# Performance work log

Hardware: AMD Instinct MI355X
Metric: run time of the kernel (lower is better)

The kernel has to match this reference:

```python
import jax, jax.numpy as jnp
import numpy as np

S = 7  # YOLOv1 grid size


def _iou(a, b):
    # a, b: [..., 4] corner boxes (x1, y1, x2, y2); eps matches global get_iou (1e-7)
    xl = jnp.maximum(a[..., 0], b[..., 0])
    yt = jnp.maximum(a[..., 1], b[..., 1])
    xr = jnp.minimum(a[..., 2], b[..., 2])
    yb = jnp.minimum(a[..., 3], b[..., 3])
    ix = jnp.maximum(xr - xl, 0.0)
    iy = jnp.maximum(yb - yt, 0.0)
    inter = ix * iy
    aa = jnp.abs((a[..., 2] - a[..., 0]) * (a[..., 3] - a[..., 1]))
    ba = jnp.abs((b[..., 2] - b[..., 0]) * (b[..., 3] - b[..., 1]))
    return inter / (aa + ba - inter + 1e-7)


def setup_inputs() -> dict:
    key = jax.random.key(0)
    k1, k2, k3 = jax.random.split(key, 3)
    N, C = 8192, 30  # 5 * num_bboxes(2) + num_classes(20)
    modely = jax.random.normal(k1, (N, S, S, C), dtype=jnp.float32)
    targety = jax.random.uniform(k2, (N, S, S, C), dtype=jnp.float32)
    # keep target wh strictly positive so sqrt(target_wh) is well-behaved
    targety = targety.at[..., 2:4].set(targety[..., 2:4] * 0.9 + 0.05)
    obj = (jax.random.uniform(k3, (N, S, S)) < 0.3).astype(jnp.float32)
    targety = targety.at[..., 4].set(obj)
    targety = targety.at[..., 9].set(obj)
    return {"modely": modely, "targety": targety}


def reference(modely, targety):
    p, t = modely, targety
    # lt_norm: meshgrid 'xy' -> lt[i, j] = (j, i) / S
    cell_x, cell_y = np.meshgrid(np.arange(S), np.arange(S))
    lt = jnp.asarray(np.dstack([cell_x, cell_y]).astype(np.float32)) / S  # [7,7,2]

    coord = (t[..., 4] > 0).astype(p.dtype)   # [N,7,7]
    noobj = (t[..., 4] == 0).astype(p.dtype)  # [N,7,7]

    # predicted box 1: corners from center-offset/size parametrization
    p_xy1 = lt + p[..., 0:2] / S - p[..., 2:4] / 2
    b1 = jnp.concatenate([p_xy1, p[..., 2:4] + p_xy1], axis=-1)
    # predicted box 2: faithfully replicates the source (uses p[...,5:7]/2, not p[...,7:9]/2)
    p_xy2 = lt + p[..., 5:7] * (1.0 / S - 0.5)
    b2 = jnp.concatenate([p_xy2, p[..., 7:9] + p_xy2], axis=-1)
    # target box
    t_xy = lt + t[..., 0:2] / S - t[..., 2:4] / 2
    tb = jnp.concatenate([t_xy, t[..., 2:4] + t_xy], axis=-1)

    iou1 = _iou(b1, tb)  # [N,7,7]
    iou2 = _iou(b2, tb)
    sel = (iou1 >= iou2)[..., None]
    # best box (raw network values, like modely[coord_mask][:, :10][high_bbox])
    box = jnp.where(sel, p[..., 0:5], p[..., 5:10])  # [N,7,7,5]

    xy_se = jnp.sum(coord * jnp.sum((box[..., 0:2] - t[..., 0:2]) ** 2, axis=-1))
    wh_p = jnp.sign(box[..., 2:4]) * jnp.sqrt(jnp.abs(box[..., 2:4]))
    wh_se = jnp.sum(coord * jnp.sum((wh_p - jnp.sqrt(t[..., 2:4])) ** 2, axis=-1))
    obj_se = jnp.sum(coord * (jnp.maximum(iou1, iou2) - box[..., 4]) ** 2)
    noobj_se = jnp.sum(noobj * ((p[..., 4] - t[..., 4]) ** 2 + (p[..., 9] - t[..., 9]) ** 2))
    label_se = jnp.sum(coord * jnp.sum((p[..., 10:] - t[..., 10:]) ** 2, axis=-1))

    loss = 5.0 * (xy_se + wh_se) + obj_se + 0.5 * noobj_se + label_se
    return loss / t.shape[0]
```

## Files before the change

kernel.cpp:

```cpp
#include <hip/hip_runtime.h>


#define NCH 30
#define CELLS_PER_SAMPLE 49

__device__ __forceinline__ float iou_f(float a0, float a1, float a2, float a3,
                                       float b0, float b1, float b2, float b3) {
    float xl = fmaxf(a0, b0);
    float yt = fmaxf(a1, b1);
    float xr = fminf(a2, b2);
    float yb = fminf(a3, b3);
    float ix = fmaxf(xr - xl, 0.0f);
    float iy = fmaxf(yb - yt, 0.0f);
    float inter = ix * iy;
    float aa = fabsf((a2 - a0) * (a3 - a1));
    float ba = fabsf((b2 - b0) * (b3 - b1));
    return inter / (aa + ba - inter + 1e-7f);
}

__device__ __forceinline__ float cell_loss_f(const float* __restrict__ pv,
                                             const float* __restrict__ tv,
                                             int cell) {
    int rem = cell % CELLS_PER_SAMPLE;
    int ci = rem / 7;
    int cj = rem % 7;

    float ltx = (float)cj / 7.0f;
    float lty = (float)ci / 7.0f;

    float coord = (tv[4] > 0.0f) ? 1.0f : 0.0f;
    float noobj = (tv[4] == 0.0f) ? 1.0f : 0.0f;

    float b1x1 = ltx + pv[0] / 7.0f - pv[2] * 0.5f;
    float b1y1 = lty + pv[1] / 7.0f - pv[3] * 0.5f;
    float b1x2 = pv[2] + b1x1;
    float b1y2 = pv[3] + b1y1;

    const float C2 = (float)(1.0 / 7.0 - 0.5);
    float b2x1 = ltx + pv[5] * C2;
    float b2y1 = lty + pv[6] * C2;
    float b2x2 = pv[7] + b2x1;
    float b2y2 = pv[8] + b2y1;

    float tbx1 = ltx + tv[0] / 7.0f - tv[2] * 0.5f;
    float tby1 = lty + tv[1] / 7.0f - tv[3] * 0.5f;
    float tbx2 = tv[2] + tbx1;
    float tby2 = tv[3] + tby1;

    float iou1 = iou_f(b1x1, b1y1, b1x2, b1y2, tbx1, tby1, tbx2, tby2);
    float iou2 = iou_f(b2x1, b2y1, b2x2, b2y2, tbx1, tby1, tbx2, tby2);

    bool sel = (iou1 >= iou2);
    float bx = sel ? pv[0] : pv[5];
    float by = sel ? pv[1] : pv[6];
    float bw = sel ? pv[2] : pv[7];
    float bh = sel ? pv[3] : pv[8];
    float bc = sel ? pv[4] : pv[9];

    float dx = bx - tv[0];
    float dy = by - tv[1];
    float xy_se = dx * dx + dy * dy;

    float sw = (bw > 0.0f) ? 1.0f : ((bw < 0.0f) ? -1.0f : 0.0f);
    float sh = (bh > 0.0f) ? 1.0f : ((bh < 0.0f) ? -1.0f : 0.0f);
    float dw = sw * sqrtf(fabsf(bw)) - sqrtf(tv[2]);
    float dh = sh * sqrtf(fabsf(bh)) - sqrtf(tv[3]);
    float wh_se = dw * dw + dh * dh;

    float mio = fmaxf(iou1, iou2);
    float dob = mio - bc;
    float obj_se = dob * dob;

    float d4 = pv[4] - tv[4];
    float d9 = pv[9] - tv[9];
    float noobj_se = d4 * d4 + d9 * d9;

    float lab = 0.0f;
    #pragma unroll
    for (int k = 10; k < NCH; ++k) {
        float d = pv[k] - tv[k];
        lab += d * d;
    }

    return coord * (5.0f * (xy_se + wh_se) + obj_se + lab)
         + 0.5f * noobj * noobj_se;
}

__global__ __launch_bounds__(256, 4) void yolo_loss_kernel(
    const float* __restrict__ p, const float* __restrict__ t,
    float* __restrict__ out, int ncells, float inv_n)
{
    const int tid  = threadIdx.x;
    const int cell = blockIdx.x * 256 + tid;

    float acc = 0.0f;
    if (cell < ncells) {
        const float2* __restrict__ pp =
            (const float2*)(p + (size_t)cell * NCH);
        const float2* __restrict__ tp =
            (const float2*)(t + (size_t)cell * NCH);

        float pv[NCH], tv[NCH];
        #pragma unroll
        for (int k = 0; k < NCH / 2; ++k) {
            float2 a = pp[k];
            float2 b = tp[k];
            pv[2 * k] = a.x; pv[2 * k + 1] = a.y;
            tv[2 * k] = b.x; tv[2 * k + 1] = b.y;
        }

        acc = cell_loss_f(pv, tv, cell) * inv_n;
    }

    #pragma unroll
    for (int off = 32; off > 0; off >>= 1)
        acc += __shfl_down(acc, off, 64);

    __shared__ float wave_sums[4];
    const int lane = tid & 63;
    const int wid  = tid >> 6;
    if (lane == 0) wave_sums[wid] = acc;
    __syncthreads();
    if (tid == 0) {
        atomicAdd(out, wave_sums[0] + wave_sums[1] + wave_sums[2] + wave_sums[3]);
    }
}

extern "C" void kernel_launch(void* const* d_in, const int* in_sizes, int n_in,
                              void* d_out, int out_size, void* d_ws, size_t ws_size,
                              hipStream_t stream) {
    const float* p = (const float*)d_in[0];
    const float* t = (const float*)d_in[1];
    float* out = (float*)d_out;

    int ncells = in_sizes[0] / NCH;
    int nsamples = ncells / CELLS_PER_SAMPLE;
    int nblocks = (ncells + 255) / 256;

    hipMemsetAsync(out, 0, sizeof(float) * (size_t)out_size, stream);

    yolo_loss_kernel<<<nblocks, 256, 0, stream>>>(
        p, t, out, ncells, 1.0f / (float)nsamples);
}
```

Measured before the change: 122.0 us.

## Stage tiles via global_load_lds double buffering in persistent blocks

After: 113.3 us. 7.1% less time.

```diff
diff --git a/kernel.cpp b/kernel.cpp
--- a/kernel.cpp
+++ b/kernel.cpp
@@ -3,6 +3,33 @@
 
 #define NCH 30
 #define CELLS_PER_SAMPLE 49
+#define TILE_CELLS 128
+#define ARR_TILE_BYTES (TILE_CELLS * NCH * 4)
+#define TILE_BYTES (2 * ARR_TILE_BYTES)
+#define NXFER 30
+#define NBLOCKS 512
+
+__device__ __forceinline__ void gl_lds16(const char* g, char* l) {
+    __builtin_amdgcn_global_load_lds(
+        (const __attribute__((address_space(1))) unsigned int*)g,
+        (__attribute__((address_space(3))) unsigned int*)l, 16, 0, 0);
+}
+
+__device__ __forceinline__ void stage_tile(const char* __restrict__ p,
+                                           const char* __restrict__ t,
+                                           int g, char* ldst, int xr, int lane) {
+    size_t base = (size_t)g * ARR_TILE_BYTES;
+    #pragma unroll
+    for (int j0 = 0; j0 < 8; ++j0) {
+        int j = xr + j0 * 4;
+        if (j < NXFER) {
+            const char* src = (j < 15)
+                ? p + base + (size_t)j * 1024 + (size_t)lane * 16
+                : t + base + (size_t)(j - 15) * 1024 + (size_t)lane * 16;
+            gl_lds16(src, ldst + j * 1024);
+        }
+    }
+}
 
 __device__ __forceinline__ float iou_f(float a0, float a1, float a2, float a3,
                                        float b0, float b1, float b2, float b3) {
@@ -86,39 +113,55 @@
          + 0.5f * noobj * noobj_se;
 }
 
-__global__ __launch_bounds__(256, 4) void yolo_loss_kernel(
-    const float* __restrict__ p, const float* __restrict__ t,
-    float* __restrict__ out, int ncells, float inv_n)
+__global__ __launch_bounds__(256, 2) void yolo_loss_kernel(
+    const char* __restrict__ p, const char* __restrict__ t,
+    float* __restrict__ out, int ntiles, float inv_n)
 {
+    __shared__ char lds[2 * TILE_BYTES];
+    __shared__ float wave_sums[4];
+
     const int tid  = threadIdx.x;
-    const int cell = blockIdx.x * 256 + tid;
+    const int lane = tid & 63;
+    const int wid  = tid >> 6;
+    const int xr = (wid + 2) & 3;
 
     float acc = 0.0f;
-    if (cell < ncells) {
-        const float2* __restrict__ pp =
-            (const float2*)(p + (size_t)cell * NCH);
-        const float2* __restrict__ tp =
-            (const float2*)(t + (size_t)cell * NCH);
+    int tile = blockIdx.x;
+    int buf = 0;
+    if (tile < ntiles) stage_tile(p, t, tile, lds, xr, lane);
 
-        float pv[NCH], tv[NCH];
-        #pragma unroll
-        for (int k = 0; k < NCH / 2; ++k) {
-            float2 a = pp[k];
-            float2 b = tp[k];
-            pv[2 * k] = a.x; pv[2 * k + 1] = a.y;
-            tv[2 * k] = b.x; tv[2 * k + 1] = b.y;
+    for (; tile < ntiles; tile += NBLOCKS) {
+        int next = tile + NBLOCKS;
+        asm volatile("s_waitcnt vmcnt(0)" ::: "memory");
+        __syncthreads();
+        if (next < ntiles)
+            stage_tile(p, t, next, lds + (buf ^ 1) * TILE_BYTES, xr, lane);
+
+        if (tid < TILE_CELLS) {
+            const float* pvp = (const float*)(lds + buf * TILE_BYTES) + tid * NCH;
+            const float* tvp = (const float*)(lds + buf * TILE_BYTES + ARR_TILE_BYTES) + tid * NCH;
+
+            float pv[NCH], tv[NCH];
+            #pragma unroll
+            for (int k = 0; k < NCH / 2; ++k) {
+                float2 a = ((const float2*)pvp)[k];
+                float2 b = ((const float2*)tvp)[k];
+                pv[2 * k] = a.x; pv[2 * k + 1] = a.y;
+                tv[2 * k] = b.x; tv[2 * k + 1] = b.y;
+            }
+
+            acc += cell_loss_f(pv, tv, tile * TILE_CELLS + tid);
         }
 
-        acc = cell_loss_f(pv, tv, cell) * inv_n;
+        buf ^= 1;
     }
+
+    acc *= inv_n;
 
     #pragma unroll
     for (int off = 32; off > 0; off >>= 1)
         acc += __shfl_down(acc, off, 64);
 
-    __shared__ float wave_sums[4];
-    const int lane = tid & 63;
-    const int wid  = tid >> 6;
     if (lane == 0) wave_sums[wid] = acc;
     __syncthreads();
     if (tid == 0) {
@@ -129,16 +172,16 @@
 extern "C" void kernel_launch(void* const* d_in, const int* in_sizes, int n_in,
                               void* d_out, int out_size, void* d_ws, size_t ws_size,
                               hipStream_t stream) {
-    const float* p = (const float*)d_in[0];
-    const float* t = (const float*)d_in[1];
+    const char* p = (const char*)d_in[0];
+    const char* t = (const char*)d_in[1];
     float* out = (float*)d_out;
 
     int ncells = in_sizes[0] / NCH;
     int nsamples = ncells / CELLS_PER_SAMPLE;
-    int nblocks = (ncells + 255) / 256;
+    int ntiles = ncells / TILE_CELLS;
 
     hipMemsetAsync(out, 0, sizeof(float) * (size_t)out_size, stream);
 
-    yolo_loss_kernel<<<nblocks, 256, 0, stream>>>(
-        p, t, out, ncells, 1.0f / (float)nsamples);
+    yolo_loss_kernel<<<NBLOCKS, 256, 0, stream>>>(
+        p, t, out, ntiles, 1.0f / (float)nsamples);
 }
```
